# Kernel tuning notes

Hardware: AMD Instinct MI355X
Metric: run time of the kernel (lower is better)

The kernel has to match this reference:

```python
import jax, jax.numpy as jnp
import numpy as np

N_NODES = 50000
N_EDGES = 600000
C_IN = 128
C_HID = 256
EPS = 1e-5  # InstanceNorm1d default eps


def setup_inputs() -> dict:
    key = jax.random.key(0)
    ks = jax.random.split(key, 12)
    node_features = jax.random.normal(ks[0], (N_NODES, C_IN), dtype=jnp.float32)
    edge_features = jax.random.normal(ks[1], (N_EDGES, C_IN), dtype=jnp.float32)
    edge_index = jax.random.randint(ks[2], (2, N_EDGES), 0, N_NODES, dtype=jnp.int64)
    s1 = 1.0 / np.sqrt(C_IN)
    s2 = 1.0 / np.sqrt(C_HID)
    # FCNN_one params (acts on summed node features)
    W1a = jax.random.uniform(ks[3], (C_IN, C_HID), jnp.float32, -s1, s1)
    b1a = jax.random.uniform(ks[4], (C_HID,), jnp.float32, -s1, s1)
    W2a = jax.random.uniform(ks[5], (C_HID, C_IN), jnp.float32, -s2, s2)
    b2a = jax.random.uniform(ks[6], (C_IN,), jnp.float32, -s2, s2)
    # FCNN_two params (acts on edge features)
    W1b = jax.random.uniform(ks[7], (C_IN, C_HID), jnp.float32, -s1, s1)
    b1b = jax.random.uniform(ks[8], (C_HID,), jnp.float32, -s1, s1)
    W2b = jax.random.uniform(ks[9], (C_HID, C_IN), jnp.float32, -s2, s2)
    b2b = jax.random.uniform(ks[10], (C_IN,), jnp.float32, -s2, s2)
    return {
        "node_features": node_features,
        "edge_features": edge_features,
        "edge_index": edge_index,
        "W1a": W1a, "b1a": b1a, "W2a": W2a, "b2a": b2a,
        "W1b": W1b, "b1b": b1b, "W2b": W2b, "b2b": b2b,
    }


def reference(node_features, edge_features, edge_index,
              W1a, b1a, W2a, b2a, W1b, b1b, W2b, b2b):
    src, dst = edge_index[0], edge_index[1]
    # gather node pairs and sum: [E, C_IN]
    s = node_features[src] + node_features[dst]
    # FCNN_one on node sums
    hn = jnp.maximum(s @ W1a + b1a, 0.0) @ W2a + b2a
    # FCNN_two on edge features
    he = jnp.maximum(edge_features @ W1b + b1b, 0.0) @ W2b + b2b
    h = hn + he  # [E, C_IN]
    # InstanceNorm1d on a (1, C) reshape == normalize each edge's feature vector
    mu = jnp.mean(h, axis=-1, keepdims=True)
    var = jnp.mean(jnp.square(h - mu), axis=-1, keepdims=True)  # biased variance
    h = (h - mu) * jax.lax.rsqrt(var + EPS)
    # dropout in eval mode = identity; relu; residual with original edge features
    return edge_features + jnp.maximum(h, 0.0)
```

## Files before the change

kernel.cpp:

```cpp
#include <hip/hip_runtime.h>
#include <stdint.h>
#include <stddef.h>

#define NE 600000
#define NN 50000
#define CI 128
#define CH 256
#define EPSI 1e-5f

typedef __attribute__((ext_vector_type(8))) short bf8;
typedef __attribute__((ext_vector_type(4))) float f4;
typedef __attribute__((ext_vector_type(4))) unsigned int u4;

union FragU { bf8 h; uint32_t w[4]; };

__device__ __forceinline__ unsigned short f2bf(float f) {
  union { float f; uint32_t u; } v; v.f = f;
  uint32_t u = v.u;
  u += 0x7FFFu + ((u >> 16) & 1u);
  return (unsigned short)(u >> 16);
}

__device__ __forceinline__ uint32_t cvtpk(float lo, float hi) {
  uint32_t r;
  asm("v_cvt_pk_bf16_f32 %0, %1, %2" : "=v"(r) : "v"(lo), "v"(hi));
  return r;
}

__device__ __forceinline__ float asf(uint32_t x) {
  union { uint32_t u; float f; } v; v.u = x; return v.f;
}

__global__ void pack_weights(const float* __restrict__ W1a, const float* __restrict__ W1b,
                             const float* __restrict__ W2a, const float* __restrict__ W2b,
                             unsigned short* __restrict__ ws) {
  int i = blockIdx.x * 256 + threadIdx.x;
  if (i >= 4 * 32768) return;
  int m = i >> 15;
  int r = i & 32767;
  int j = r & 7;
  int l = (r >> 3) & 63;
  int kg = l >> 4, q = l & 15;
  float val;
  if (m < 2) {
    int t = (r >> 9) & 3;
    int tau = (r >> 11) & 1;
    int c = (r >> 12) & 7;
    int cin = 32 * t + kg * 8 + j;
    int hid = 32 * c + 8 * (q >> 2) + 4 * tau + (q & 3);
    const float* W1 = (m == 0) ? W1a : W1b;
    val = W1[cin * CH + hid];
  } else {
    int c = (r >> 9) & 7;
    int mt = (r >> 12) & 7;
    int hid = 32 * c + kg * 8 + j;
    int cout = 16 * mt + q;
    const float* W2 = (m == 2) ? W2a : W2b;
    val = W2[hid * CI + cout];
  }
  ws[(size_t)m * 32768 + r] = f2bf(val);
}

__global__ __launch_bounds__(256)
void node_pre(const float* __restrict__ node, const float* __restrict__ b1a,
              const unsigned short* __restrict__ wp, unsigned short* __restrict__ Ua) {
  const int tid = threadIdx.x;
  const int lane = tid & 63;
  const int wv = tid >> 6;
  const int kg = lane >> 4, ar = lane & 15;
  const int n0 = blockIdx.x * 64 + wv * 16 + ar;
  const bool okn = (n0 < NN);
  const int n = okn ? n0 : (NN - 1);
  const float* pn = node + (size_t)n * CI;

  FragU xn[4];
#pragma unroll
  for (int t = 0; t < 4; ++t) {
    const int c0 = t * 32 + kg * 8;
    f4 v0 = *(const f4*)(pn + c0);
    f4 v1 = *(const f4*)(pn + c0 + 4);
    xn[t].w[0] = cvtpk(v0[0], v0[1]); xn[t].w[1] = cvtpk(v0[2], v0[3]);
    xn[t].w[2] = cvtpk(v1[0], v1[1]); xn[t].w[3] = cvtpk(v1[2], v1[3]);
  }
  const int lofs = lane * 8;
#pragma unroll 1
  for (int c = 0; c < 8; ++c) {
    f4 t0 = *(const f4*)(b1a + c * 32 + kg * 8) * 0.5f;
    f4 t1 = *(const f4*)(b1a + c * 32 + kg * 8 + 4) * 0.5f;
    const unsigned short* p1 = wp + c * 4096;
#pragma unroll
    for (int t = 0; t < 4; ++t) {
      bf8 a0 = *(const bf8*)(p1 + t * 512 + lofs);
      bf8 a1 = *(const bf8*)(p1 + 2048 + t * 512 + lofs);
      t0 = __builtin_amdgcn_mfma_f32_16x16x32_bf16(a0, xn[t].h, t0, 0, 0, 0);
      t1 = __builtin_amdgcn_mfma_f32_16x16x32_bf16(a1, xn[t].h, t1, 0, 0, 0);
    }
    u4 q;
    q[0] = cvtpk(t0[0], t0[1]); q[1] = cvtpk(t0[2], t0[3]);
    q[2] = cvtpk(t1[0], t1[1]); q[3] = cvtpk(t1[2], t1[3]);
    if (okn) *(u4*)(Ua + (size_t)n * CH + c * 32 + kg * 8) = q;
  }
}

#define ISSUE(Sv, Dv, u) \
  Sv = *(const u4*)(pUs + (u) * 32 + kg * 8); \
  Dv = *(const u4*)(pUd + (u) * 32 + kg * 8);

#define DENSE(c) { \
  f4 t0 = *(const f4*)(b1b + (c) * 32 + kg * 8); \
  f4 t1 = *(const f4*)(b1b + (c) * 32 + kg * 8 + 4); \
  _Pragma("unroll") \
  for (int t = 0; t < 4; ++t) { \
    bf8 a0 = *(const bf8*)(lw + (c) * 4096 + t * 512 + lofs); \
    bf8 a1 = *(const bf8*)(lw + (c) * 4096 + 2048 + t * 512 + lofs); \
    t0 = __builtin_amdgcn_mfma_f32_16x16x32_bf16(a0, xe[t].h, t0, 0, 0, 0); \
    t1 = __builtin_amdgcn_mfma_f32_16x16x32_bf16(a1, xe[t].h, t1, 0, 0, 0); \
  } \
  FragU bf_; \
  bf_.w[0] = cvtpk(fmaxf(t0[0], 0.f), fmaxf(t0[1], 0.f)); \
  bf_.w[1] = cvtpk(fmaxf(t0[2], 0.f), fmaxf(t0[3], 0.f)); \
  bf_.w[2] = cvtpk(fmaxf(t1[0], 0.f), fmaxf(t1[1], 0.f)); \
  bf_.w[3] = cvtpk(fmaxf(t1[2], 0.f), fmaxf(t1[3], 0.f)); \
  _Pragma("unroll") \
  for (int mt = 0; mt < 8; ++mt) { \
    bf8 a2 = *(const bf8*)(lw + 32768 + (mt * 8 + (c)) * 512 + lofs); \
    hacc[mt] = __builtin_amdgcn_mfma_f32_16x16x32_bf16(a2, bf_.h, hacc[mt], 0, 0, 0); \
  } }

#define CONS(Sv, Dv, u) { \
  FragU tb; \
  _Pragma("unroll") \
  for (int i = 0; i < 4; ++i) { \
    float lo = asf(Sv[i] << 16) + asf(Dv[i] << 16); \
    float hi = asf(Sv[i] & 0xFFFF0000u) + asf(Dv[i] & 0xFFFF0000u); \
    tb.w[i] = cvtpk(fmaxf(lo, 0.f), fmaxf(hi, 0.f)); \
  } \
  _Pragma("unroll") \
  for (int mt = 0; mt < 8; ++mt) { \
    bf8 aW = *(const bf8*)(P2a + (mt * 8 + (u)) * 512 + lofs); \
    hacc[mt] = __builtin_amdgcn_mfma_f32_16x16x32_bf16(aW, tb.h, hacc[mt], 0, 0, 0); \
  } }

__global__ __launch_bounds__(1024, 4)
void edge_fused(const unsigned short* __restrict__ Ua,
                const float* __restrict__ ef,
                const int* __restrict__ eidx,
                const float* __restrict__ b1b,
                const float* __restrict__ b2a, const float* __restrict__ b2b,
                const unsigned short* __restrict__ wp,
                float* __restrict__ out) {
  __shared__ __align__(16) unsigned short lw[65536];
  const int tid = threadIdx.x;
  const int lane = tid & 63;
  const int wv = tid >> 6;
  const int kg = lane >> 4, ar = lane & 15;
  const int lofs = lane * 8;

  const int e = blockIdx.x * 256 + wv * 16 + ar;
  const int ec = (e < NE) ? e : (NE - 1);
  const int is = eidx[ec], id = eidx[NE + ec];
  const unsigned short* pUs = Ua + (size_t)is * CH;
  const unsigned short* pUd = Ua + (size_t)id * CH;
  const unsigned short* P2a = wp + 65536;

  {
    const u4* s1 = (const u4*)(wp + 32768);
    const u4* s2 = (const u4*)(wp + 98304);
    u4* l = (u4*)lw;
#pragma unroll
    for (int i = 0; i < 4; ++i) {
      int o = i * 1024 + tid;
      l[o] = s1[o];
      l[4096 + o] = s2[o];
    }
  }

  const float* pe = ef + (size_t)ec * CI;
  FragU xe[4];
#pragma unroll
  for (int t = 0; t < 4; ++t) {
    const int c0 = t * 32 + kg * 8;
    f4 v0 = *(const f4*)(pe + c0);
    f4 v1 = *(const f4*)(pe + c0 + 4);
    xe[t].w[0] = cvtpk(v0[0], v0[1]); xe[t].w[1] = cvtpk(v0[2], v0[3]);
    xe[t].w[2] = cvtpk(v1[0], v1[1]); xe[t].w[3] = cvtpk(v1[2], v1[3]);
  }

  f4 hacc[8];
#pragma unroll
  for (int mt = 0; mt < 8; ++mt) {
    f4 u = *(const f4*)(b2a + mt * 16 + kg * 4);
    f4 v = *(const f4*)(b2b + mt * 16 + kg * 4);
    hacc[mt] = u + v;
  }

  __syncthreads();

  u4 As, Ad, Bs, Bd;
  ISSUE(As, Ad, 0)
  ISSUE(Bs, Bd, 1)
  DENSE(0) CONS(As, Ad, 0) ISSUE(As, Ad, 2)
  DENSE(1) CONS(Bs, Bd, 1) ISSUE(Bs, Bd, 3)
  DENSE(2) CONS(As, Ad, 2) ISSUE(As, Ad, 4)
  DENSE(3) CONS(Bs, Bd, 3) ISSUE(Bs, Bd, 5)
  DENSE(4) CONS(As, Ad, 4) ISSUE(As, Ad, 6)
  DENSE(5) CONS(Bs, Bd, 5) ISSUE(Bs, Bd, 7)
  DENSE(6) CONS(As, Ad, 6)
  DENSE(7) CONS(Bs, Bd, 7)

  {
    float sum = 0.f, sq = 0.f;
#pragma unroll
    for (int mt = 0; mt < 8; ++mt)
#pragma unroll
      for (int i = 0; i < 4; ++i) { float v = hacc[mt][i]; sum += v; sq += v * v; }
    sum += __shfl_xor(sum, 16); sum += __shfl_xor(sum, 32);
    sq  += __shfl_xor(sq, 16);  sq  += __shfl_xor(sq, 32);
    const float mu = sum * (1.0f / 128.0f);
    const float var = sq * (1.0f / 128.0f) - mu * mu;
    const float rs = rsqrtf(var + EPSI);
    if (e < NE) {
      float* po = out + (size_t)e * CI;
      const float* pr = ef + (size_t)e * CI;
#pragma unroll
      for (int mt = 0; mt < 8; ++mt) {
        f4 r = *(const f4*)(pr + mt * 16 + kg * 4);
        f4 o;
#pragma unroll
        for (int i = 0; i < 4; ++i) {
          float n = (hacc[mt][i] - mu) * rs;
          o[i] = r[i] + fmaxf(n, 0.f);
        }
        *(f4*)(po + mt * 16 + kg * 4) = o;
      }
    }
  }
}

extern "C" void kernel_launch(void* const* d_in, const int* in_sizes, int n_in,
                              void* d_out, int out_size, void* d_ws, size_t ws_size,
                              hipStream_t stream) {
  const float* node = (const float*)d_in[0];
  const float* ef   = (const float*)d_in[1];
  const int* eidx   = (const int*)d_in[2];
  const float* W1a = (const float*)d_in[3];
  const float* b1a = (const float*)d_in[4];
  const float* W2a = (const float*)d_in[5];
  const float* b2a = (const float*)d_in[6];
  const float* W1b = (const float*)d_in[7];
  const float* b1b = (const float*)d_in[8];
  const float* W2b = (const float*)d_in[9];
  const float* b2b = (const float*)d_in[10];
  unsigned short* wp = (unsigned short*)d_ws;
  unsigned short* Ua = wp + 131072;
  float* outp = (float*)d_out;

  pack_weights<<<512, 256, 0, stream>>>(W1a, W1b, W2a, W2b, wp);
  node_pre<<<(NN + 63) / 64, 256, 0, stream>>>(node, b1a, wp, Ua);
  edge_fused<<<(NE + 255) / 256, 1024, 0, stream>>>(
      Ua, ef, eidx, b1b, b2a, b2b, wp, outp);
}
```

Before: 369.6 us.

## Counting-sort edges by source node and reuse bf16 edge features from LDS

Adds a counting sort of edges by source node (zero, histogram with atomics, single-block scan, atomic scatter) so edge blocks gather Ua rows with better locality. It also remaps block IDs across the 8 XCDs. In the epilogue, the residual comes from the bf16 edge-feature fragments parked in LDS instead of re-reading fp32 edge features from global memory. The cost is four extra launches, including a serial single-block scan, and an edge-ordered rather than contiguous pattern for edge-feature loads and output writes. Taking the residual from bf16 also loses precision in the output.

```diff
diff --git a/kernel.cpp b/kernel.cpp
--- a/kernel.cpp
+++ b/kernel.cpp
@@ -11,6 +11,7 @@
 typedef __attribute__((ext_vector_type(8))) short bf8;
 typedef __attribute__((ext_vector_type(4))) float f4;
 typedef __attribute__((ext_vector_type(4))) unsigned int u4;
+typedef __attribute__((ext_vector_type(2))) unsigned int u2;
 
 union FragU { bf8 h; uint32_t w[4]; };
 
@@ -102,6 +103,47 @@
   }
 }
 
+__global__ void zero_cnt(int* cnt) {
+  int i = blockIdx.x * 256 + threadIdx.x;
+  if (i < 50048) cnt[i] = 0;
+}
+__global__ void hist_src(const int* __restrict__ eidx, int* __restrict__ cnt) {
+  int e = blockIdx.x * 256 + threadIdx.x;
+  if (e < NE) atomicAdd(cnt + eidx[e], 1);
+}
+__global__ __launch_bounds__(1024)
+void scan_cnt(int* cnt) {
+  __shared__ int part[1024];
+  const int tid = threadIdx.x;
+  const int CPT = (NN + 1023) / 1024;
+  const int base = tid * CPT;
+  int s = 0;
+  for (int i = 0; i < CPT; ++i) { int idx = base + i; if (idx < NN) s += cnt[idx]; }
+  part[tid] = s;
+  __syncthreads();
+  for (int off = 1; off < 1024; off <<= 1) {
+    int v = (tid >= off) ? part[tid - off] : 0;
+    __syncthreads();
+    part[tid] += v;
+    __syncthreads();
+  }
+  int excl = (tid == 0) ? 0 : part[tid - 1];
+  for (int i = 0; i < CPT; ++i) {
+    int idx = base + i;
+    if (idx < NN) { int c = cnt[idx]; cnt[idx] = excl; excl += c; }
+  }
+}
+__global__ void scatter_edges(const int* __restrict__ eidx, int* __restrict__ offs,
+                              int* __restrict__ sSrc, int* __restrict__ sDst,
+                              int* __restrict__ sEid) {
+  int e = blockIdx.x * 256 + threadIdx.x;
+  if (e < NE) {
+    int s = eidx[e];
+    int p = atomicAdd(offs + s, 1);
+    sSrc[p] = s; sDst[p] = eidx[NE + e]; sEid[p] = e;
+  }
+}
+
 #define ISSUE(Sv, Dv, u) \
   Sv = *(const u4*)(pUs + (u) * 32 + kg * 8); \
   Dv = *(const u4*)(pUd + (u) * 32 + kg * 8);
@@ -148,7 +190,9 @@
                 const float* __restrict__ b1b,
                 const float* __restrict__ b2a, const float* __restrict__ b2b,
                 const unsigned short* __restrict__ wp,
-                float* __restrict__ out) {
+                float* __restrict__ out,
+                const int* __restrict__ sSrc, const int* __restrict__ sDst,
+                const int* __restrict__ sEid) {
   __shared__ __align__(16) unsigned short lw[65536];
   const int tid = threadIdx.x;
   const int lane = tid & 63;
@@ -156,9 +200,15 @@
   const int kg = lane >> 4, ar = lane & 15;
   const int lofs = lane * 8;
 
-  const int e = blockIdx.x * 256 + wv * 16 + ar;
-  const int ec = (e < NE) ? e : (NE - 1);
-  const int is = eidx[ec], id = eidx[NE + ec];
+  int bid = blockIdx.x;
+  const int nb = gridDim.x;
+  if ((nb & 7) == 0) { int q = nb >> 3; bid = (bid & 7) * q + (bid >> 3); }
+
+  const int p = bid * 256 + wv * 16 + ar;
+  const int pc = (p < NE) ? p : (NE - 1);
+  int e, is, id;
+  if (sEid) { is = sSrc[pc]; id = sDst[pc]; e = sEid[pc]; }
+  else      { e = pc; is = eidx[pc]; id = eidx[NE + pc]; }
   const unsigned short* pUs = Ua + (size_t)is * CH;
   const unsigned short* pUd = Ua + (size_t)id * CH;
   const unsigned short* P2a = wp + 65536;
@@ -175,7 +225,7 @@
     }
   }
 
-  const float* pe = ef + (size_t)ec * CI;
+  const float* pe = ef + (size_t)e * CI;
   FragU xe[4];
 #pragma unroll
   for (int t = 0; t < 4; ++t) {
@@ -208,6 +258,15 @@
   DENSE(6) CONS(As, Ad, 6)
   DENSE(7) CONS(Bs, Bd, 7)
 
+  __syncthreads();
+  const int row = wv * 16 + ar;
+  const int sx = (row & 7) << 4;
+#pragma unroll
+  for (int t = 0; t < 4; ++t) {
+    u4 vv = {xe[t].w[0], xe[t].w[1], xe[t].w[2], xe[t].w[3]};
+    *(u4*)((char*)lw + ((row * 256 + t * 64 + kg * 16) ^ sx)) = vv;
+  }
+
   {
     float sum = 0.f, sq = 0.f;
 #pragma unroll
@@ -219,18 +278,16 @@
     const float mu = sum * (1.0f / 128.0f);
     const float var = sq * (1.0f / 128.0f) - mu * mu;
     const float rs = rsqrtf(var + EPSI);
-    if (e < NE) {
+    if (p < NE) {
       float* po = out + (size_t)e * CI;
-      const float* pr = ef + (size_t)e * CI;
 #pragma unroll
       for (int mt = 0; mt < 8; ++mt) {
-        f4 r = *(const f4*)(pr + mt * 16 + kg * 4);
+        u2 rv = *(const u2*)((char*)lw + ((row * 256 + mt * 32 + kg * 8) ^ sx));
         f4 o;
-#pragma unroll
-        for (int i = 0; i < 4; ++i) {
-          float n = (hacc[mt][i] - mu) * rs;
-          o[i] = r[i] + fmaxf(n, 0.f);
-        }
+        o[0] = asf(rv[0] << 16)          + fmaxf((hacc[mt][0] - mu) * rs, 0.f);
+        o[1] = asf(rv[0] & 0xFFFF0000u)  + fmaxf((hacc[mt][1] - mu) * rs, 0.f);
+        o[2] = asf(rv[1] << 16)          + fmaxf((hacc[mt][2] - mu) * rs, 0.f);
+        o[3] = asf(rv[1] & 0xFFFF0000u)  + fmaxf((hacc[mt][3] - mu) * rs, 0.f);
         *(f4*)(po + mt * 16 + kg * 4) = o;
       }
     }
@@ -255,8 +312,24 @@
   unsigned short* Ua = wp + 131072;
   float* outp = (float*)d_out;
 
+  int* cnt  = (int*)((char*)d_ws + 262144 + (size_t)NN * CH * 2);
+  int* sSrc = cnt + 50048;
+  int* sDst = sSrc + NE;
+  int* sEid = sDst + NE;
+  const size_t need = 262144 + (size_t)NN * CH * 2 + 4u * (50048 + 3 * NE);
+  const bool use_sort = (ws_size >= need);
+
   pack_weights<<<512, 256, 0, stream>>>(W1a, W1b, W2a, W2b, wp);
   node_pre<<<(NN + 63) / 64, 256, 0, stream>>>(node, b1a, wp, Ua);
-  edge_fused<<<(NE + 255) / 256, 1024, 0, stream>>>(
-      Ua, ef, eidx, b1b, b2a, b2b, wp, outp);
-}
+  if (use_sort) {
+    zero_cnt<<<196, 256, 0, stream>>>(cnt);
+    hist_src<<<(NE + 255) / 256, 256, 0, stream>>>(eidx, cnt);
+    scan_cnt<<<1, 1024, 0, stream>>>(cnt);
+    scatter_edges<<<(NE + 255) / 256, 256, 0, stream>>>(eidx, cnt, sSrc, sDst, sEid);
+    edge_fused<<<(NE + 255) / 256, 1024, 0, stream>>>(
+        Ua, ef, eidx, b1b, b2a, b2b, wp, outp, sSrc, sDst, sEid);
+  } else {
+    edge_fused<<<(NE + 255) / 256, 1024, 0, stream>>>(
+        Ua, ef, eidx, b1b, b2a, b2b, wp, outp, nullptr, nullptr, nullptr);
+  }
+}
```

New measurement: 498.5 us. 34.9% more time.
